# Optimization experiments

Measured on AMD Instinct MI355X. Metric: run time of the kernel, lower is better.

Reference implementation:

```python
import jax, jax.numpy as jnp
import numpy as np

NUM_EMBEDDINGS = 512
EMBEDDING_DIM = 64
COMMITMENT_COST = 0.25


def setup_inputs() -> dict:
    key = jax.random.key(0)
    k1, k2 = jax.random.split(key)
    inputs = jax.random.normal(k1, (16, 16384, EMBEDDING_DIM), dtype=jnp.float32)
    # torch init: uniform_(-1/num_embeddings, 1/num_embeddings)
    embedding = jax.random.uniform(
        k2, (NUM_EMBEDDINGS, EMBEDDING_DIM), dtype=jnp.float32,
        minval=-1.0 / NUM_EMBEDDINGS, maxval=1.0 / NUM_EMBEDDINGS)
    return {"inputs": inputs, "embedding": embedding}


def reference(inputs, embedding):
    K, D = embedding.shape
    flat = inputs.reshape(-1, D)  # [N, D]
    distances = (jnp.sum(flat * flat, axis=1, keepdims=True)
                 + jnp.sum(embedding * embedding, axis=1)
                 - 2.0 * (flat @ embedding.T))
    encoding_indices = jnp.argmin(distances, axis=1)  # [N]
    encodings = jax.nn.one_hot(encoding_indices, K, dtype=inputs.dtype)  # [N, K]
    # one-hot @ codebook == gather
    quantized = jnp.take(embedding, encoding_indices, axis=0).reshape(inputs.shape)
    e_latent_loss = jnp.mean((jax.lax.stop_gradient(quantized) - inputs) ** 2)
    q_latent_loss = jnp.mean((quantized - jax.lax.stop_gradient(inputs)) ** 2)
    vq_loss = q_latent_loss + COMMITMENT_COST * e_latent_loss
    # straight-through estimator
    quantized_st = inputs + jax.lax.stop_gradient(quantized - inputs)
    avg_probs = jnp.mean(encodings, axis=0)
    perplexity = jnp.exp(-jnp.sum(avg_probs * jnp.log(avg_probs + 1e-10)))
    return (vq_loss, quantized_st, perplexity, encodings, encoding_indices)
```

## Files before the change

### kernel.cpp

```cpp
#include <hip/hip_runtime.h>
#include <math.h>

#define N_ROWS (16 * 16384)
#define D 64
#define K 512
#define BLOCK 256
#define RPT 2
#define ROWS_PER_BLOCK (BLOCK * RPT)
#define GRID (N_ROWS / ROWS_PER_BLOCK)
#define CHUNK 128
#define NCHUNK (K / CHUNK)

#define OFF_LOSS 0ULL
#define OFF_Q    1ULL
#define OFF_PERP (1ULL + (unsigned long long)N_ROWS * D)
#define OFF_ENC  (OFF_PERP + 1ULL)
#define OFF_IDX  (OFF_ENC + (unsigned long long)N_ROWS * K)

__global__ __launch_bounds__(BLOCK)
__attribute__((amdgpu_waves_per_eu(2, 2)))
void vq_main(
    const float* __restrict__ x, const float* __restrict__ emb,
    float* __restrict__ out, float* __restrict__ ws_loss,
    unsigned int* __restrict__ ws_hist)
{
    __shared__ float lds_e[CHUNK * D];
    __shared__ float lds_se[K];
    __shared__ unsigned int lds_hist[K];
    __shared__ float lds_red[BLOCK / 64];

    const int tid = threadIdx.x;
    const int bid = blockIdx.x;
    const int row0 = bid * ROWS_PER_BLOCK + tid;
    const int row1 = row0 + BLOCK;

    lds_hist[tid] = 0;
    lds_hist[tid + BLOCK] = 0;

    for (int k = tid; k < K; k += BLOCK) {
        const float4* e4 = (const float4*)(emb + (size_t)k * D);
        float s = 0.f;
        #pragma unroll
        for (int i = 0; i < 16; i++) {
            float4 e = e4[i];
            s = fmaf(e.x, e.x, s); s = fmaf(e.y, e.y, s);
            s = fmaf(e.z, e.z, s); s = fmaf(e.w, e.w, s);
        }
        lds_se[k] = s;
    }

    float4 xa[16], xb[16];
    {
        const float4* pa = (const float4*)(x + (size_t)row0 * D);
        const float4* pb = (const float4*)(x + (size_t)row1 * D);
        #pragma unroll
        for (int i = 0; i < 16; i++) { xa[i] = pa[i]; xb[i] = pb[i]; }
    }

    float sxa, sxb;
    {
        float4 sa = make_float4(0.f, 0.f, 0.f, 0.f);
        float4 sb = make_float4(0.f, 0.f, 0.f, 0.f);
        #pragma unroll
        for (int i = 0; i < 16; i++) {
            sa.x = fmaf(xa[i].x, xa[i].x, sa.x);
            sa.y = fmaf(xa[i].y, xa[i].y, sa.y);
            sa.z = fmaf(xa[i].z, xa[i].z, sa.z);
            sa.w = fmaf(xa[i].w, xa[i].w, sa.w);
            sb.x = fmaf(xb[i].x, xb[i].x, sb.x);
            sb.y = fmaf(xb[i].y, xb[i].y, sb.y);
            sb.z = fmaf(xb[i].z, xb[i].z, sb.z);
            sb.w = fmaf(xb[i].w, xb[i].w, sb.w);
        }
        sxa = (sa.x + sa.y) + (sa.z + sa.w);
        sxb = (sb.x + sb.y) + (sb.z + sb.w);
    }

    float2* encb = (float2*)(out + OFF_ENC + (size_t)bid * ROWS_PER_BLOCK * K);
    const float2 z2 = make_float2(0.f, 0.f);

    float bestA = __builtin_inff(), bestB = __builtin_inff();
    int bkA = 0, bkB = 0;

    for (int c = 0; c < NCHUNK; c++) {
        __syncthreads();
        {
            const float4* src = (const float4*)(emb + (size_t)c * CHUNK * D);
            float4* dst = (float4*)lds_e;
            #pragma unroll
            for (int i = 0; i < 8; i++) dst[i * BLOCK + tid] = src[i * BLOCK + tid];
        }
        __syncthreads();

        #pragma unroll 2
        for (int kk = 0; kk < CHUNK; kk++) {
            const int k = c * CHUNK + kk;
            encb[(size_t)k * BLOCK + tid] = z2;

            const float4* ev = (const float4*)(lds_e + kk * D);
            float4 a0 = make_float4(0.f, 0.f, 0.f, 0.f);
            float4 a1 = make_float4(0.f, 0.f, 0.f, 0.f);
            #pragma unroll
            for (int i = 0; i < 16; i++) {
                float4 e = ev[i];
                a0.x = fmaf(xa[i].x, e.x, a0.x);
                a0.y = fmaf(xa[i].y, e.y, a0.y);
                a0.z = fmaf(xa[i].z, e.z, a0.z);
                a0.w = fmaf(xa[i].w, e.w, a0.w);
                a1.x = fmaf(xb[i].x, e.x, a1.x);
                a1.y = fmaf(xb[i].y, e.y, a1.y);
                a1.z = fmaf(xb[i].z, e.z, a1.z);
                a1.w = fmaf(xb[i].w, e.w, a1.w);
            }
            float dot0 = (a0.x + a0.y) + (a0.z + a0.w);
            float dot1 = (a1.x + a1.y) + (a1.z + a1.w);
            float se = lds_se[k];
            float d0 = fmaf(-2.0f, dot0, sxa + se);
            float d1 = fmaf(-2.0f, dot1, sxb + se);
            if (d0 < bestA) { bestA = d0; bkA = k; }
            if (d1 < bestB) { bestB = d1; bkB = k; }
        }
    }

    out[OFF_IDX + (size_t)row0] = (float)bkA;
    out[OFF_IDX + (size_t)row1] = (float)bkB;

    float loss = 0.f;
    {
        const float4* ea = (const float4*)(emb + (size_t)bkA * D);
        float* q = out + OFF_Q + (size_t)row0 * D;
        #pragma unroll
        for (int i = 0; i < 16; i++) {
            float4 e = ea[i];
            q[i * 4 + 0] = e.x; q[i * 4 + 1] = e.y;
            q[i * 4 + 2] = e.z; q[i * 4 + 3] = e.w;
            float d0 = e.x - xa[i].x, d1 = e.y - xa[i].y;
            float d2 = e.z - xa[i].z, d3 = e.w - xa[i].w;
            loss = fmaf(d0, d0, loss); loss = fmaf(d1, d1, loss);
            loss = fmaf(d2, d2, loss); loss = fmaf(d3, d3, loss);
        }
        const float4* eb = (const float4*)(emb + (size_t)bkB * D);
        q = out + OFF_Q + (size_t)row1 * D;
        #pragma unroll
        for (int i = 0; i < 16; i++) {
            float4 e = eb[i];
            q[i * 4 + 0] = e.x; q[i * 4 + 1] = e.y;
            q[i * 4 + 2] = e.z; q[i * 4 + 3] = e.w;
            float d0 = e.x - xb[i].x, d1 = e.y - xb[i].y;
            float d2 = e.z - xb[i].z, d3 = e.w - xb[i].w;
            loss = fmaf(d0, d0, loss); loss = fmaf(d1, d1, loss);
            loss = fmaf(d2, d2, loss); loss = fmaf(d3, d3, loss);
        }
    }

    for (int off = 32; off; off >>= 1) loss += __shfl_down(loss, off, 64);
    const int wave = tid >> 6, lane = tid & 63;
    if (lane == 0) lds_red[wave] = loss;
    atomicAdd(&lds_hist[bkA], 1u);
    atomicAdd(&lds_hist[bkB], 1u);
    __syncthreads();
    if (tid == 0) {
        float s = 0.f;
        for (int w = 0; w < BLOCK / 64; w++) s += lds_red[w];
        atomicAdd(ws_loss, s);
    }
    atomicAdd(&ws_hist[tid], lds_hist[tid]);
    atomicAdd(&ws_hist[tid + BLOCK], lds_hist[tid + BLOCK]);

    out[OFF_ENC + (size_t)bid * ROWS_PER_BLOCK * K + (size_t)tid * K + (size_t)bkA] = 1.0f;
    out[OFF_ENC + (size_t)bid * ROWS_PER_BLOCK * K + (size_t)(tid + BLOCK) * K + (size_t)bkB] = 1.0f;
}

__global__ __launch_bounds__(K) void vq_finalize(
    const unsigned int* __restrict__ ws_hist,
    const float* __restrict__ ws_loss, float* __restrict__ out)
{
    __shared__ float red[K / 64];
    const int tid = threadIdx.x;
    float p = (float)ws_hist[tid] * (1.0f / (float)N_ROWS);
    float s = p * logf(p + 1e-10f);
    for (int off = 32; off; off >>= 1) s += __shfl_down(s, off, 64);
    if ((tid & 63) == 0) red[tid >> 6] = s;
    __syncthreads();
    if (tid == 0) {
        float t = 0.f;
        for (int w = 0; w < K / 64; w++) t += red[w];
        out[OFF_PERP] = expf(-t);
        float m = ws_loss[0] * (1.0f / (float)(N_ROWS * D));
        out[OFF_LOSS] = m + 0.25f * m;
    }
}

extern "C" void kernel_launch(void* const* d_in, const int* in_sizes, int n_in,
                              void* d_out, int out_size, void* d_ws, size_t ws_size,
                              hipStream_t stream)
{
    const float* x   = (const float*)d_in[0];
    const float* emb = (const float*)d_in[1];
    float* out = (float*)d_out;
    float* ws_loss = (float*)d_ws;
    unsigned int* ws_hist = (unsigned int*)d_ws + 16;

    hipMemsetAsync(d_ws, 0, 64 + K * 4, stream);
    vq_main<<<GRID, BLOCK, 0, stream>>>(x, emb, out, ws_loss, ws_hist);
    vq_finalize<<<1, K, 0, stream>>>(ws_hist, ws_loss, out);
}
```

Baseline: 848.8 us.

## Read codebook rows via scalar loads instead of staging through LDS

```diff
diff --git a/kernel.cpp b/kernel.cpp
--- a/kernel.cpp
+++ b/kernel.cpp
@@ -8,14 +8,29 @@
 #define RPT 2
 #define ROWS_PER_BLOCK (BLOCK * RPT)
 #define GRID (N_ROWS / ROWS_PER_BLOCK)
-#define CHUNK 128
-#define NCHUNK (K / CHUNK)
 
 #define OFF_LOSS 0ULL
 #define OFF_Q    1ULL
 #define OFF_PERP (1ULL + (unsigned long long)N_ROWS * D)
 #define OFF_ENC  (OFF_PERP + 1ULL)
 #define OFF_IDX  (OFF_ENC + (unsigned long long)N_ROWS * K)
+
+typedef float f32x16 __attribute__((ext_vector_type(16)));
+
+#define FMA_I(EV, II, XI) do {                                   \
+    const float ex_ = (EV)[4*(II)+0];                            \
+    const float ey_ = (EV)[4*(II)+1];                            \
+    const float ez_ = (EV)[4*(II)+2];                            \
+    const float ew_ = (EV)[4*(II)+3];                            \
+    a0.x = fmaf(xa[XI].x, ex_, a0.x);                            \
+    a0.y = fmaf(xa[XI].y, ey_, a0.y);                            \
+    a0.z = fmaf(xa[XI].z, ez_, a0.z);                            \
+    a0.w = fmaf(xa[XI].w, ew_, a0.w);                            \
+    a1.x = fmaf(xb[XI].x, ex_, a1.x);                            \
+    a1.y = fmaf(xb[XI].y, ey_, a1.y);                            \
+    a1.z = fmaf(xb[XI].z, ez_, a1.z);                            \
+    a1.w = fmaf(xb[XI].w, ew_, a1.w);                            \
+} while (0)
 
 __global__ __launch_bounds__(BLOCK)
 __attribute__((amdgpu_waves_per_eu(2, 2)))
@@ -24,7 +39,6 @@
     float* __restrict__ out, float* __restrict__ ws_loss,
     unsigned int* __restrict__ ws_hist)
 {
-    __shared__ float lds_e[CHUNK * D];
     __shared__ float lds_se[K];
     __shared__ unsigned int lds_hist[K];
     __shared__ float lds_red[BLOCK / 64];
@@ -76,50 +90,47 @@
         sxb = (sb.x + sb.y) + (sb.z + sb.w);
     }
 
+    __syncthreads();
+
     float2* encb = (float2*)(out + OFF_ENC + (size_t)bid * ROWS_PER_BLOCK * K);
     const float2 z2 = make_float2(0.f, 0.f);
 
     float bestA = __builtin_inff(), bestB = __builtin_inff();
     int bkA = 0, bkB = 0;
 
-    for (int c = 0; c < NCHUNK; c++) {
-        __syncthreads();
-        {
-            const float4* src = (const float4*)(emb + (size_t)c * CHUNK * D);
-            float4* dst = (float4*)lds_e;
-            #pragma unroll
-            for (int i = 0; i < 8; i++) dst[i * BLOCK + tid] = src[i * BLOCK + tid];
-        }
-        __syncthreads();
-
-        #pragma unroll 2
-        for (int kk = 0; kk < CHUNK; kk++) {
-            const int k = c * CHUNK + kk;
-            encb[(size_t)k * BLOCK + tid] = z2;
-
-            const float4* ev = (const float4*)(lds_e + kk * D);
-            float4 a0 = make_float4(0.f, 0.f, 0.f, 0.f);
-            float4 a1 = make_float4(0.f, 0.f, 0.f, 0.f);
-            #pragma unroll
-            for (int i = 0; i < 16; i++) {
-                float4 e = ev[i];
-                a0.x = fmaf(xa[i].x, e.x, a0.x);
-                a0.y = fmaf(xa[i].y, e.y, a0.y);
-                a0.z = fmaf(xa[i].z, e.z, a0.z);
-                a0.w = fmaf(xa[i].w, e.w, a0.w);
-                a1.x = fmaf(xb[i].x, e.x, a1.x);
-                a1.y = fmaf(xb[i].y, e.y, a1.y);
-                a1.z = fmaf(xb[i].z, e.z, a1.z);
-                a1.w = fmaf(xb[i].w, e.w, a1.w);
-            }
-            float dot0 = (a0.x + a0.y) + (a0.z + a0.w);
-            float dot1 = (a1.x + a1.y) + (a1.z + a1.w);
-            float se = lds_se[k];
-            float d0 = fmaf(-2.0f, dot0, sxa + se);
-            float d1 = fmaf(-2.0f, dot1, sxb + se);
-            if (d0 < bestA) { bestA = d0; bkA = k; }
-            if (d1 < bestB) { bestB = d1; bkB = k; }
-        }
+    #pragma unroll 1
+    for (int k = 0; k < K; k++) {
+        encb[(size_t)k * BLOCK + tid] = z2;
+
+        const float* ep = emb + (size_t)k * D;
+        f32x16 e0, e1, e2, e3;
+        asm volatile(
+            "s_load_dwordx16 %0, %4, 0x0\n\t"
+            "s_load_dwordx16 %1, %4, 0x40\n\t"
+            "s_load_dwordx16 %2, %4, 0x80\n\t"
+            "s_load_dwordx16 %3, %4, 0xC0\n\t"
+            "s_waitcnt lgkmcnt(0)"
+            : "=s"(e0), "=s"(e1), "=s"(e2), "=s"(e3)
+            : "s"(ep));
+
+        float4 a0 = make_float4(0.f, 0.f, 0.f, 0.f);
+        float4 a1 = make_float4(0.f, 0.f, 0.f, 0.f);
+        #pragma unroll
+        for (int i = 0; i < 4; i++) FMA_I(e0, i, i);
+        #pragma unroll
+        for (int i = 0; i < 4; i++) FMA_I(e1, i, 4 + i);
+        #pragma unroll
+        for (int i = 0; i < 4; i++) FMA_I(e2, i, 8 + i);
+        #pragma unroll
+        for (int i = 0; i < 4; i++) FMA_I(e3, i, 12 + i);
+
+        float dot0 = (a0.x + a0.y) + (a0.z + a0.w);
+        float dot1 = (a1.x + a1.y) + (a1.z + a1.w);
+        float se = lds_se[k];
+        float d0 = fmaf(-2.0f, dot0, sxa + se);
+        float d1 = fmaf(-2.0f, dot1, sxb + se);
+        if (d0 < bestA) { bestA = d0; bkA = k; }
+        if (d1 < bestB) { bestB = d1; bkB = k; }
     }
 
     out[OFF_IDX + (size_t)row0] = (float)bkA;
```

After: 881.9 us. 3.9% more time.
